# Optimization experiments

Measured on AMD Instinct MI355X. Metric: run time of the kernel, lower is better.

The kernel has to match this reference:

```python
import jax, jax.numpy as jnp
import numpy as np

N = 4096      # nodes
F = 512       # nfeat
D = 64        # nhid per head
H = 8         # nheads
C = 40        # nclass
ALPHA = 0.2   # leakyrelu slope
NEG = -1e9    # mask value (finite for bf16/fp16 safety; exp -> 0)
EDGE_P = 0.004


def setup_inputs() -> dict:
    key = jax.random.key(0)
    ks = jax.random.split(key, 8)
    x = jax.random.normal(ks[0], (N, F), jnp.float32)
    adj = jax.random.uniform(ks[1], (N, N)) < EDGE_P
    adj = adj | jnp.eye(N, dtype=bool)  # self-loops: every softmax row valid
    init = lambda k, shape, fan: jax.random.normal(k, shape, jnp.float32) / np.sqrt(fan)
    W1 = init(ks[2], (H, F, D), F)        # per-head tran.weight^T
    a1_src = init(ks[3], (H, D), D)       # att1 (j / source term)
    a1_dst = init(ks[4], (H, D), D)       # att2 (i / destination term)
    W2 = init(ks[5], (H * D, C), H * D)   # output head tran
    a2_src = init(ks[6], (C,), C)
    a2_dst = init(ks[7], (C,), C)
    return dict(x=x, adj=adj, W1=W1, a1_src=a1_src, a1_dst=a1_dst,
                W2=W2, a2_src=a2_src, a2_dst=a2_dst)


def reference(x, adj, W1, a1_src, a1_dst, W2, a2_src, a2_dst):
    # ---- layer 1: H heads in parallel (dropout = identity in eval) ----
    h = jnp.einsum('nf,hfd->hnd', x, W1)              # [H,N,D]
    si = jnp.einsum('hnd,hd->hn', h, a1_dst)          # att2(h): i term
    sj = jnp.einsum('hnd,hd->hn', h, a1_src)          # att1(h): j term
    e = jax.nn.leaky_relu(si[:, :, None] + sj[:, None, :], ALPHA)  # [H,N,N]
    e = jnp.where(adj[None], e, NEG)                  # mask non-edges
    p = jax.nn.softmax(e, axis=-1)                    # softmax over neighbors j
    out = jnp.einsum('hij,hjd->hid', p, h)            # [H,N,D]
    # torch.cat(heads, dim=1) -> [N, H*D] with heads contiguous
    x2 = jax.nn.elu(jnp.transpose(out, (1, 0, 2)).reshape(N, H * D))
    # ---- output attention head ----
    h2 = x2 @ W2                                      # [N,C]
    e2 = jax.nn.leaky_relu((h2 @ a2_dst)[:, None] + (h2 @ a2_src)[None, :], ALPHA)
    e2 = jnp.where(adj, e2, NEG)
    p2 = jax.nn.softmax(e2, axis=-1)
    return p2 @ h2                                    # [N,C]
```

## Files before the change

kernel.cpp:

```cpp
#include <hip/hip_runtime.h>

#define NN 4096
#define FF 512
#define DD 64
#define HH 8
#define CC 40
#define HD (HH * DD)
#define CP 64
#define MAXDEG 128
#define ALPHA 0.2f

#define BM 64
#define BN 64
#define BK 16
#define SK2 8
#define KH2 (FF / SK2)

typedef __attribute__((ext_vector_type(8))) short bf16x8;
typedef __attribute__((ext_vector_type(4))) float f32x4;

__device__ __forceinline__ float bf2f(unsigned short u) {
    union { unsigned int i; float f; } v;
    v.i = ((unsigned int)u) << 16;
    return v.f;
}

__device__ __forceinline__ unsigned short f2bf(float f) {
    union { float f; unsigned int u; } v;
    v.f = f;
    unsigned int r = v.u + 0x7fffu + ((v.u >> 16) & 1u);
    return (unsigned short)(r >> 16);
}

__device__ __forceinline__ float wave_sum(float v) {
    #pragma unroll
    for (int off = 32; off; off >>= 1) v += __shfl_xor(v, off, 64);
    return v;
}

__device__ __forceinline__ float wave_max(float v) {
    #pragma unroll
    for (int off = 32; off; off >>= 1) v = fmaxf(v, __shfl_xor(v, off, 64));
    return v;
}

__device__ __forceinline__ float read_f(const void* src, int i, int isBf16) {
    if (isBf16) return bf2f(((const unsigned short*)src)[i]);
    return ((const float*)src)[i];
}

__device__ __forceinline__ int sniff_x(const void* xraw, int tid, int* fS) {
    if (tid == 0) *fS = 1;
    __syncthreads();
    int bad = 0;
    const unsigned int* xw = (const unsigned int*)xraw;
    #pragma unroll
    for (int q = 0; q < 4; q++) {
        unsigned int w = xw[(tid & 255) * 4 + q];
        unsigned int e0 = (w >> 7) & 0xffu;
        unsigned int e1 = (w >> 23) & 0xffu;
        if (e0 >= 0x90u || e1 >= 0x90u) bad = 1;
    }
    if (bad) *fS = 0;
    __syncthreads();
    return *fS;
}

__global__ __launch_bounds__(256) void cvt_all(const void* __restrict__ x,
                                               const void* __restrict__ W1,
                                               const void* __restrict__ W2,
                                               const void* __restrict__ a1s,
                                               const void* __restrict__ a1d,
                                               const void* __restrict__ a2s,
                                               const void* __restrict__ a2d,
                                               unsigned short* __restrict__ W1bth,
                                               unsigned short* __restrict__ W1btl,
                                               float* __restrict__ W2p,
                                               float* __restrict__ a1sf,
                                               float* __restrict__ a1df,
                                               float* __restrict__ a2sf,
                                               float* __restrict__ a2df,
                                               float* __restrict__ si,
                                               float* __restrict__ sj) {
    __shared__ int fS;
    int bf = sniff_x(x, threadIdx.x, &fS);
    int i = blockIdx.x * 256 + threadIdx.x;
    const int nW1 = HH * FF * DD;
    const int nW2p = HD * CP;
    const int nA1 = HD;
    const int nSS = HH * NN;
    if (i < nW1) {
        int hd = i / (FF * DD);
        int rem = i % (FF * DD);
        int f = rem / DD, d = rem % DD;
        float v = read_f(W1, i, bf);
        unsigned short h16 = f2bf(v);
        int idx = (hd * DD + d) * FF + f;
        W1bth[idx] = h16;
        W1btl[idx] = f2bf(v - bf2f(h16));
        return;
    }
    i -= nW1;
    if (i < nW2p) {
        int k = i / CP, c = i % CP;
        W2p[i] = (c < CC) ? read_f(W2, k * CC + c, bf) : 0.f;
        return;
    }
    i -= nW2p;
    if (i < nA1) { a1sf[i] = read_f(a1s, i, bf); return; }
    i -= nA1;
    if (i < nA1) { a1df[i] = read_f(a1d, i, bf); return; }
    i -= nA1;
    if (i < CC) { a2sf[i] = read_f(a2s, i, bf); return; }
    i -= CC;
    if (i < CC) { a2df[i] = read_f(a2d, i, bf); return; }
    i -= CC;
    if (i < nSS) { si[i] = 0.f; return; }
    i -= nSS;
    if (i < nSS) { sj[i] = 0.f; return; }
}

__global__ __launch_bounds__(256) void build_nbr(const unsigned char* __restrict__ adj,
                                                 int* __restrict__ nbr,
                                                 int* __restrict__ deg) {
    __shared__ int cnt;
    __shared__ int fS;
    if (threadIdx.x == 0) { cnt = 0; fS = 1; }
    __syncthreads();
    if (adj[(size_t)threadIdx.x * (NN + 1)] == 0) fS = 0;
    __syncthreads();
    int isByte = fS;
    int i = blockIdx.x;
    if (isByte) {
        uint4 v = ((const uint4*)(adj + (size_t)i * NN))[threadIdx.x];
        unsigned int u[4] = { v.x, v.y, v.z, v.w };
        int base = threadIdx.x * 16;
        #pragma unroll
        for (int q = 0; q < 4; q++) {
            #pragma unroll
            for (int b = 0; b < 4; b++) {
                if ((u[q] >> (8 * b)) & 0xffu) {
                    int p = atomicAdd(&cnt, 1);
                    if (p < MAXDEG) nbr[(size_t)i * MAXDEG + p] = base + q * 4 + b;
                }
            }
        }
    } else {
        const int4* row = (const int4*)((const int*)adj + (size_t)i * NN);
        #pragma unroll
        for (int q = 0; q < 4; q++) {
            int idx4 = q * 256 + threadIdx.x;
            int4 v = row[idx4];
            int base = idx4 * 4;
            if (v.x) { int p = atomicAdd(&cnt, 1); if (p < MAXDEG) nbr[(size_t)i * MAXDEG + p] = base; }
            if (v.y) { int p = atomicAdd(&cnt, 1); if (p < MAXDEG) nbr[(size_t)i * MAXDEG + p] = base + 1; }
            if (v.z) { int p = atomicAdd(&cnt, 1); if (p < MAXDEG) nbr[(size_t)i * MAXDEG + p] = base + 2; }
            if (v.w) { int p = atomicAdd(&cnt, 1); if (p < MAXDEG) nbr[(size_t)i * MAXDEG + p] = base + 3; }
        }
    }
    __syncthreads();
    if (threadIdx.x == 0) deg[i] = min(cnt, MAXDEG);
}

__global__ __launch_bounds__(256) void l1_gemm(const void* __restrict__ xraw,
                                               const unsigned short* __restrict__ W1bth,
                                               const unsigned short* __restrict__ W1btl,
                                               const float* __restrict__ a1sf,
                                               const float* __restrict__ a1df,
                                               unsigned short* __restrict__ hb,
                                               float* __restrict__ si,
                                               float* __restrict__ sj) {
    __shared__ __align__(16) unsigned short Ah[64][40];
    __shared__ __align__(16) unsigned short Al[64][40];
    __shared__ __align__(16) unsigned short Bh[64][40];
    __shared__ __align__(16) unsigned short Bl[64][40];
    __shared__ int fS;

    int bm = blockIdx.x, hd = blockIdx.y;
    int tid = threadIdx.x;
    int isBf16 = sniff_x(xraw, tid, &fS);

    int wave = tid >> 6, lane = tid & 63;
    int wm = wave >> 1, wn = wave & 1;
    int lr = lane & 15, lg = lane >> 4;
    int srow = tid >> 2;
    int sseg = (tid & 3) * 8;

    const unsigned short* wAp = W1bth + (size_t)(hd * 64 + srow) * FF + sseg;
    const unsigned short* wBp = W1btl + (size_t)(hd * 64 + srow) * FF + sseg;

    f32x4 acc[2][2];
    #pragma unroll
    for (int r = 0; r < 2; r++)
        #pragma unroll
        for (int c = 0; c < 2; c++) acc[r][c] = (f32x4){0.f, 0.f, 0.f, 0.f};

    if (isBf16) {
        const unsigned short* xp = (const unsigned short*)xraw
                                 + (size_t)(bm * 64 + srow) * FF + sseg;
        uint4 ra = *(const uint4*)xp;
        uint4 rb = *(const uint4*)wAp;
        for (int kk = 0; kk < FF; kk += 32) {
            __syncthreads();
            *(uint4*)&Ah[srow][sseg] = ra;
            *(uint4*)&Bh[srow][sseg] = rb;
            __syncthreads();
            int kn = (kk + 32 < FF) ? kk + 32 : kk;
            ra = *(const uint4*)(xp + kn);
            rb = *(const uint4*)(wAp + kn);
            bf16x8 a0 = *(const bf16x8*)&Ah[wm * 32 + lr][lg * 8];
            bf16x8 a1 = *(const bf16x8*)&Ah[wm * 32 + 16 + lr][lg * 8];
            bf16x8 b0 = *(const bf16x8*)&Bh[wn * 32 + lr][lg * 8];
            bf16x8 b1 = *(const bf16x8*)&Bh[wn * 32 + 16 + lr][lg * 8];
            acc[0][0] = __builtin_amdgcn_mfma_f32_16x16x32_bf16(a0, b0, acc[0][0], 0, 0, 0);
            acc[0][1] = __builtin_amdgcn_mfma_f32_16x16x32_bf16(a0, b1, acc[0][1], 0, 0, 0);
            acc[1][0] = __builtin_amdgcn_mfma_f32_16x16x32_bf16(a1, b0, acc[1][0], 0, 0, 0);
            acc[1][1] = __builtin_amdgcn_mfma_f32_16x16x32_bf16(a1, b1, acc[1][1], 0, 0, 0);
        }
    } else {
        const float* xp = (const float*)xraw + (size_t)(bm * 64 + srow) * FF + sseg;
        float4 ra0 = *(const float4*)xp;
        float4 ra1 = *(const float4*)(xp + 4);
        uint4 rbh = *(const uint4*)wAp;
        uint4 rbl = *(const uint4*)wBp;
        for (int kk = 0; kk < FF; kk += 32) {
            __syncthreads();
            union { unsigned short s[8]; uint4 v; } uh, ul;
            float fv[8] = { ra0.x, ra0.y, ra0.z, ra0.w, ra1.x, ra1.y, ra1.z, ra1.w };
            #pragma unroll
            for (int q = 0; q < 8; q++) {
                unsigned short h16 = f2bf(fv[q]);
                uh.s[q] = h16;
                ul.s[q] = f2bf(fv[q] - bf2f(h16));
            }
            *(uint4*)&Ah[srow][sseg] = uh.v;
            *(uint4*)&Al[srow][sseg] = ul.v;
            *(uint4*)&Bh[srow][sseg] = rbh;
            *(uint4*)&Bl[srow][sseg] = rbl;
            __syncthreads();
            int kn = (kk + 32 < FF) ? kk + 32 : kk;
            ra0 = *(const float4*)(xp + kn);
            ra1 = *(const float4*)(xp + kn + 4);
            rbh = *(const uint4*)(wAp + kn);
            rbl = *(const uint4*)(wBp + kn);

            bf16x8 a_h0 = *(const bf16x8*)&Ah[wm * 32 + lr][lg * 8];
            bf16x8 a_h1 = *(const bf16x8*)&Ah[wm * 32 + 16 + lr][lg * 8];
            bf16x8 a_l0 = *(const bf16x8*)&Al[wm * 32 + lr][lg * 8];
            bf16x8 a_l1 = *(const bf16x8*)&Al[wm * 32 + 16 + lr][lg * 8];
            bf16x8 b_h0 = *(const bf16x8*)&Bh[wn * 32 + lr][lg * 8];
            bf16x8 b_h1 = *(const bf16x8*)&Bh[wn * 32 + 16 + lr][lg * 8];
            bf16x8 b_l0 = *(const bf16x8*)&Bl[wn * 32 + lr][lg * 8];
            bf16x8 b_l1 = *(const bf16x8*)&Bl[wn * 32 + 16 + lr][lg * 8];

            acc[0][0] = __builtin_amdgcn_mfma_f32_16x16x32_bf16(a_h0, b_h0, acc[0][0], 0, 0, 0);
            acc[0][1] = __builtin_amdgcn_mfma_f32_16x16x32_bf16(a_h0, b_h1, acc[0][1], 0, 0, 0);
            acc[1][0] = __builtin_amdgcn_mfma_f32_16x16x32_bf16(a_h1, b_h0, acc[1][0], 0, 0, 0);
            acc[1][1] = __builtin_amdgcn_mfma_f32_16x16x32_bf16(a_h1, b_h1, acc[1][1], 0, 0, 0);
            acc[0][0] = __builtin_amdgcn_mfma_f32_16x16x32_bf16(a_h0, b_l0, acc[0][0], 0, 0, 0);
            acc[0][1] = __builtin_amdgcn_mfma_f32_16x16x32_bf16(a_h0, b_l1, acc[0][1], 0, 0, 0);
            acc[1][0] = __builtin_amdgcn_mfma_f32_16x16x32_bf16(a_h1, b_l0, acc[1][0], 0, 0, 0);
            acc[1][1] = __builtin_amdgcn_mfma_f32_16x16x32_bf16(a_h1, b_l1, acc[1][1], 0, 0, 0);
            acc[0][0] = __builtin_amdgcn_mfma_f32_16x16x32_bf16(a_l0, b_h0, acc[0][0], 0, 0, 0);
            acc[0][1] = __builtin_amdgcn_mfma_f32_16x16x32_bf16(a_l0, b_h1, acc[0][1], 0, 0, 0);
            acc[1][0] = __builtin_amdgcn_mfma_f32_16x16x32_bf16(a_l1, b_h0, acc[1][0], 0, 0, 0);
            acc[1][1] = __builtin_amdgcn_mfma_f32_16x16x32_bf16(a_l1, b_h1, acc[1][1], 0, 0, 0);
        }
    }

    float adv[2], asv[2];
    #pragma unroll
    for (int fc = 0; fc < 2; fc++) {
        adv[fc] = a1df[hd * DD + wn * 32 + fc * 16 + lr];
        asv[fc] = a1sf[hd * DD + wn * 32 + fc * 16 + lr];
    }
    #pragma unroll
    for (int fr = 0; fr < 2; fr++) {
        #pragma unroll
        for (int q = 0; q < 4; q++) {
            int row = bm * 64 + wm * 32 + fr * 16 + lg * 4 + q;
            int colb = hd * 64 + wn * 32;
            hb[(size_t)row * HD + colb + lr] = f2bf(acc[fr][0][q]);
            hb[(size_t)row * HD + colb + 16 + lr] = f2bf(acc[fr][1][q]);
            float pd = acc[fr][0][q] * adv[0] + acc[fr][1][q] * adv[1];
            float ps = acc[fr][0][q] * asv[0] + acc[fr][1][q] * asv[1];
            #pragma unroll
            for (int off = 1; off < 16; off <<= 1) {
                pd += __shfl_xor(pd, off, 64);
                ps += __shfl_xor(ps, off, 64);
            }
            if (lr == 0) {
                atomicAdd(&si[hd * NN + row], pd);
                atomicAdd(&sj[hd * NN + row], ps);
            }
        }
    }
}

__global__ __launch_bounds__(256) void l1_attn(const int* __restrict__ nbr,
                                               const int* __restrict__ deg,
                                               const unsigned short* __restrict__ hb,
                                               const float* __restrict__ si,
                                               const float* __restrict__ sj,
                                               float* __restrict__ x2) {
    int i = blockIdx.x;
    int tid = threadIdx.x;
    int wave = tid >> 6, lane = tid & 63;
    int d = deg[i];
    __shared__ int js[MAXDEG];
    __shared__ float wls[HH][MAXDEG];
    for (int k = tid; k < d; k += 256) js[k] = nbr[(size_t)i * MAXDEG + k];
    __syncthreads();

    int hd = wave * 2 + (lane >> 5);
    int l32 = lane & 31;
    float sii = si[hd * NN + i];
    const float* sjh = sj + (size_t)hd * NN;
    float m = -1e30f;
    for (int k = l32; k < d; k += 32) {
        float sc = sii + sjh[js[k]];
        sc = sc > 0.f ? sc : ALPHA * sc;
        wls[hd][k] = sc;
        m = fmaxf(m, sc);
    }
    #pragma unroll
    for (int off = 16; off; off >>= 1) m = fmaxf(m, __shfl_xor(m, off, 64));
    float s = 0.f;
    for (int k = l32; k < d; k += 32) {
        float e = expf(wls[hd][k] - m);
        wls[hd][k] = e;
        s += e;
    }
    #pragma unroll
    for (int off = 16; off; off >>= 1) s += __shfl_xor(s, off, 64);
    float inv = 1.f / fmaxf(s, 1e-30f);
    for (int k = l32; k < d; k += 32) wls[hd][k] *= inv;
    __syncthreads();

    const unsigned int* hu = (const unsigned int*)hb;
    const float* wl = wls[tid >> 5];
    float a0 = 0.f, a1 = 0.f;
    int k = 0;
    for (; k + 4 <= d; k += 4) {
        unsigned int v0 = hu[(size_t)js[k] * 256 + tid];
        unsigned int v1 = hu[(size_t)js[k + 1] * 256 + tid];
        unsigned int v2 = hu[(size_t)js[k + 2] * 256 + tid];
        unsigned int v3 = hu[(size_t)js[k + 3] * 256 + tid];
        float w0 = wl[k], w1 = wl[k + 1], w2 = wl[k + 2], w3 = wl[k + 3];
        a0 = fmaf(w0, bf2f((unsigned short)v0), a0);
        a1 = fmaf(w0, bf2f((unsigned short)(v0 >> 16)), a1);
        a0 = fmaf(w1, bf2f((unsigned short)v1), a0);
        a1 = fmaf(w1, bf2f((unsigned short)(v1 >> 16)), a1);
        a0 = fmaf(w2, bf2f((unsigned short)v2), a0);
        a1 = fmaf(w2, bf2f((unsigned short)(v2 >> 16)), a1);
        a0 = fmaf(w3, bf2f((unsigned short)v3), a0);
        a1 = fmaf(w3, bf2f((unsigned short)(v3 >> 16)), a1);
    }
    for (; k < d; k++) {
        unsigned int v = hu[(size_t)js[k] * 256 + tid];
        float w = wl[k];
        a0 = fmaf(w, bf2f((unsigned short)v), a0);
        a1 = fmaf(w, bf2f((unsigned short)(v >> 16)), a1);
    }
    float r0 = a0 > 0.f ? a0 : expm1f(a0);
    float r1 = a1 > 0.f ? a1 : expm1f(a1);
    *(float2*)(x2 + (size_t)i * HD + tid * 2) = make_float2(r0, r1);
}

template <int KHs, int Nb>
__device__ __forceinline__ void gemm_body(const float* __restrict__ Ap,
                                          const float* __restrict__ Bp,
                                          float* __restrict__ Co,
                                          int tid, int bm) {
    __shared__ float As[BK][BM + 4];
    __shared__ float Bs[BK][BN + 4];
    int tm = tid >> 4, tn = tid & 15;
    int m0 = tm * 4, n0 = tn * 4;
    int ar = tid >> 2, ak = (tid & 3) * 4;
    int bk = tid >> 4, bq = (tid & 15) * 4;

    float acc[4][4];
    #pragma unroll
    for (int r = 0; r < 4; r++)
        #pragma unroll
        for (int c = 0; c < 4; c++) acc[r][c] = 0.f;

    const float* Ar = Ap + (size_t)ar * FF;
    float4 av = *(const float4*)(Ar + ak);
    float4 bv = *(const float4*)(Bp + (size_t)bk * Nb + bq);

    for (int k0 = 0; k0 < KHs; k0 += BK) {
        __syncthreads();
        As[ak + 0][ar] = av.x;
        As[ak + 1][ar] = av.y;
        As[ak + 2][ar] = av.z;
        As[ak + 3][ar] = av.w;
        *(float4*)&Bs[bk][bq] = bv;
        __syncthreads();

        int kn = (k0 + BK < KHs) ? k0 + BK : k0;
        av = *(const float4*)(Ar + kn + ak);
        bv = *(const float4*)(Bp + (size_t)(kn + bk) * Nb + bq);

        #pragma unroll
        for (int k = 0; k < BK; k++) {
            float4 a = *(const float4*)&As[k][m0];
            float4 b = *(const float4*)&Bs[k][n0];
            acc[0][0] = fmaf(a.x, b.x, acc[0][0]);
            acc[0][1] = fmaf(a.x, b.y, acc[0][1]);
            acc[0][2] = fmaf(a.x, b.z, acc[0][2]);
            acc[0][3] = fmaf(a.x, b.w, acc[0][3]);
            acc[1][0] = fmaf(a.y, b.x, acc[1][0]);
            acc[1][1] = fmaf(a.y, b.y, acc[1][1]);
            acc[1][2] = fmaf(a.y, b.z, acc[1][2]);
            acc[1][3] = fmaf(a.y, b.w, acc[1][3]);
            acc[2][0] = fmaf(a.z, b.x, acc[2][0]);
            acc[2][1] = fmaf(a.z, b.y, acc[2][1]);
            acc[2][2] = fmaf(a.z, b.z, acc[2][2]);
            acc[2][3] = fmaf(a.z, b.w, acc[2][3]);
            acc[3][0] = fmaf(a.w, b.x, acc[3][0]);
            acc[3][1] = fmaf(a.w, b.y, acc[3][1]);
            acc[3][2] = fmaf(a.w, b.z, acc[3][2]);
            acc[3][3] = fmaf(a.w, b.w, acc[3][3]);
        }
    }

    #pragma unroll
    for (int r = 0; r < 4; r++) {
        float4 v = make_float4(acc[r][0], acc[r][1], acc[r][2], acc[r][3]);
        *(float4*)(Co + (size_t)(bm * BM + m0 + r) * Nb + n0) = v;
    }
}

__global__ __launch_bounds__(256) void l2_gemm(const float* __restrict__ x2,
                                               const float* __restrict__ W2p,
                                               float* __restrict__ Cp2) {
    int bm = blockIdx.x, sk = blockIdx.z;
    gemm_body<KH2, CP>(x2 + (size_t)bm * BM * FF + sk * KH2,
                       W2p + (size_t)(sk * KH2) * CP,
                       Cp2 + (size_t)sk * NN * CP,
                       threadIdx.x, bm);
}

__global__ __launch_bounds__(64) void l2_post(const float* __restrict__ Cp2,
                                              const float* __restrict__ a2sf,
                                              const float* __restrict__ a2df,
                                              float* __restrict__ h2,
                                              float* __restrict__ d1,
                                              float* __restrict__ d2) {
    int n = blockIdx.x, c = threadIdx.x;
    float v = 0.f;
    #pragma unroll
    for (int sk = 0; sk < SK2; sk++)
        v += Cp2[(size_t)sk * NN * CP + (size_t)n * CP + c];
    if (c < CC) h2[(size_t)n * CC + c] = v;
    float pd = wave_sum((c < CC) ? v * a2df[c] : 0.f);
    float ps = wave_sum((c < CC) ? v * a2sf[c] : 0.f);
    if (c == 0) {
        d1[n] = pd;
        d2[n] = ps;
    }
}

__global__ __launch_bounds__(256) void l2_attn(const int* __restrict__ nbr,
                                               const int* __restrict__ deg,
                                               const float* __restrict__ h2,
                                               const float* __restrict__ d1,
                                               const float* __restrict__ d2,
                                               float* __restrict__ out) {
    int w = threadIdx.x >> 6, lane = threadIdx.x & 63;
    int i = blockIdx.x * 4 + w;
    int d = deg[i];
    __shared__ int js[4][MAXDEG];
    __shared__ float wls[4][MAXDEG];
    for (int k = lane; k < d; k += 64) js[w][k] = nbr[(size_t)i * MAXDEG + k];

    float sii = d1[i];
    float m = -1e30f;
    for (int k = lane; k < d; k += 64) {
        float sc = sii + d2[js[w][k]];
        sc = sc > 0.f ? sc : ALPHA * sc;
        wls[w][k] = sc;
        m = fmaxf(m, sc);
    }
    m = wave_max(m);
    float s = 0.f;
    for (int k = lane; k < d; k += 64) {
        float e = expf(wls[w][k] - m);
        wls[w][k] = e;
        s += e;
    }
    s = fmaxf(wave_sum(s), 1e-30f);

    int c = lane;
    if (c < CC) {
        float acc = 0.f;
        int k = 0;
        for (; k + 4 <= d; k += 4) {
            float v0 = h2[(size_t)js[w][k] * CC + c];
            float v1 = h2[(size_t)js[w][k + 1] * CC + c];
            float v2 = h2[(size_t)js[w][k + 2] * CC + c];
            float v3 = h2[(size_t)js[w][k + 3] * CC + c];
            acc = fmaf(wls[w][k], v0, acc);
            acc = fmaf(wls[w][k + 1], v1, acc);
            acc = fmaf(wls[w][k + 2], v2, acc);
            acc = fmaf(wls[w][k + 3], v3, acc);
        }
        for (; k < d; k++)
            acc = fmaf(wls[w][k], h2[(size_t)js[w][k] * CC + c], acc);
        out[(size_t)i * CC + c] = acc / s;
    }
}

extern "C" void kernel_launch(void* const* d_in, const int* in_sizes, int n_in,
                              void* d_out, int out_size, void* d_ws, size_t ws_size,
                              hipStream_t stream) {
    const void* x   = d_in[0];
    const unsigned char* adj = (const unsigned char*)d_in[1];
    const void* W1  = d_in[2];
    const void* a1s = d_in[3];
    const void* a1d = d_in[4];
    const void* W2  = d_in[5];
    const void* a2s = d_in[6];
    const void* a2d = d_in[7];

    char* ws = (char*)d_ws;
    int*   nbr   = (int*)(ws + 0);
    int*   deg   = (int*)(ws + 2097152);
    float* si    = (float*)(ws + 2113536);
    float* sj    = (float*)(ws + 2244608);
    unsigned short* W1bth = (unsigned short*)(ws + 2375680);
    unsigned short* W1btl = (unsigned short*)(ws + 2899968);
    float* W2p   = (float*)(ws + 3424256);
    float* a1sf  = (float*)(ws + 3555328);
    float* a1df  = (float*)(ws + 3557376);
    float* a2sf  = (float*)(ws + 3559424);
    float* a2df  = (float*)(ws + 3559680);
    unsigned short* hb = (unsigned short*)(ws + 3559936);
    float* x2    = (float*)(ws + 7754240);
    float* h2    = (float*)(ws + 16142848);
    float* d1    = (float*)(ws + 16798208);
    float* d2    = (float*)(ws + 16814592);
    float* Cp2   = (float*)(ws + 16830976);

    const int nCvt = HH * FF * DD + HD * CP + 2 * HD + 2 * CC + 2 * HH * NN;
    hipLaunchKernelGGL(cvt_all, dim3((nCvt + 255) / 256), dim3(256), 0, stream,
                       x, W1, W2, a1s, a1d, a2s, a2d,
                       W1bth, W1btl, W2p, a1sf, a1df, a2sf, a2df, si, sj);

    hipLaunchKernelGGL(build_nbr, dim3(NN), dim3(256), 0, stream, adj, nbr, deg);
    hipLaunchKernelGGL(l1_gemm, dim3(NN / 64, HH), dim3(256), 0, stream,
                       x, W1bth, W1btl, a1sf, a1df, hb, si, sj);
    hipLaunchKernelGGL(l1_attn, dim3(NN), dim3(256), 0, stream,
                       nbr, deg, hb, si, sj, x2);
    hipLaunchKernelGGL(l2_gemm, dim3(NN / BM, 1, SK2), dim3(256), 0, stream,
                       x2, W2p, Cp2);
    hipLaunchKernelGGL(l2_post, dim3(NN), dim3(64), 0, stream,
                       Cp2, a2sf, a2df, h2, d1, d2);
    hipLaunchKernelGGL(l2_attn, dim3(NN / 4), dim3(256), 0, stream,
                       nbr, deg, h2, d1, d2, (float*)d_out);
}
```

Measured before the change: 166.5 us.

## Merge conversion and neighbor-build kernels; replace si/sj atomics with LDS reduction

Merges the weight-conversion kernel and the adjacency neighbor-list kernel into one prep launch. The W1 transpose-split is reorganized so each thread handles 16 contiguous output features. In the layer-1 GEMM epilogue, the two column-wave partial dot products are combined through shared memory and written directly, replacing global atomics. This also removes the need to zero si/sj. The aims are to cut a launch, drop the zero-fill work and avoid atomic traffic, at the cost of an extra block barrier and a more varied prep grid.

```diff
diff --git a/kernel.cpp b/kernel.cpp
--- a/kernel.cpp
+++ b/kernel.cpp
@@ -66,41 +66,94 @@
     return *fS;
 }
 
-__global__ __launch_bounds__(256) void cvt_all(const void* __restrict__ x,
-                                               const void* __restrict__ W1,
-                                               const void* __restrict__ W2,
-                                               const void* __restrict__ a1s,
-                                               const void* __restrict__ a1d,
-                                               const void* __restrict__ a2s,
-                                               const void* __restrict__ a2d,
-                                               unsigned short* __restrict__ W1bth,
-                                               unsigned short* __restrict__ W1btl,
-                                               float* __restrict__ W2p,
-                                               float* __restrict__ a1sf,
-                                               float* __restrict__ a1df,
-                                               float* __restrict__ a2sf,
-                                               float* __restrict__ a2df,
-                                               float* __restrict__ si,
-                                               float* __restrict__ sj) {
+__global__ __launch_bounds__(256) void prep(const unsigned char* __restrict__ adj,
+                                            const void* __restrict__ x,
+                                            const void* __restrict__ W1,
+                                            const void* __restrict__ W2,
+                                            const void* __restrict__ a1s,
+                                            const void* __restrict__ a1d,
+                                            const void* __restrict__ a2s,
+                                            const void* __restrict__ a2d,
+                                            int* __restrict__ nbr,
+                                            int* __restrict__ deg,
+                                            unsigned short* __restrict__ W1bth,
+                                            unsigned short* __restrict__ W1btl,
+                                            float* __restrict__ W2p,
+                                            float* __restrict__ a1sf,
+                                            float* __restrict__ a1df,
+                                            float* __restrict__ a2sf,
+                                            float* __restrict__ a2df) {
+    __shared__ int cnt;
     __shared__ int fS;
-    int bf = sniff_x(x, threadIdx.x, &fS);
-    int i = blockIdx.x * 256 + threadIdx.x;
-    const int nW1 = HH * FF * DD;
+    int t = threadIdx.x;
+    int blk = blockIdx.x;
+
+    if (blk < NN) {
+        if (t == 0) { cnt = 0; fS = 1; }
+        __syncthreads();
+        if (adj[(size_t)t * (NN + 1)] == 0) fS = 0;
+        __syncthreads();
+        int isByte = fS;
+        int i = blk;
+        if (isByte) {
+            uint4 v = ((const uint4*)(adj + (size_t)i * NN))[t];
+            unsigned int u[4] = { v.x, v.y, v.z, v.w };
+            int base = t * 16;
+            #pragma unroll
+            for (int q = 0; q < 4; q++) {
+                #pragma unroll
+                for (int b = 0; b < 4; b++) {
+                    if ((u[q] >> (8 * b)) & 0xffu) {
+                        int p = atomicAdd(&cnt, 1);
+                        if (p < MAXDEG) nbr[(size_t)i * MAXDEG + p] = base + q * 4 + b;
+                    }
+                }
+            }
+        } else {
+            const int4* row = (const int4*)((const int*)adj + (size_t)i * NN);
+            #pragma unroll
+            for (int q = 0; q < 4; q++) {
+                int idx4 = q * 256 + t;
+                int4 v = row[idx4];
+                int base = idx4 * 4;
+                if (v.x) { int p = atomicAdd(&cnt, 1); if (p < MAXDEG) nbr[(size_t)i * MAXDEG + p] = base; }
+                if (v.y) { int p = atomicAdd(&cnt, 1); if (p < MAXDEG) nbr[(size_t)i * MAXDEG + p] = base + 1; }
+                if (v.z) { int p = atomicAdd(&cnt, 1); if (p < MAXDEG) nbr[(size_t)i * MAXDEG + p] = base + 2; }
+                if (v.w) { int p = atomicAdd(&cnt, 1); if (p < MAXDEG) nbr[(size_t)i * MAXDEG + p] = base + 3; }
+            }
+        }
+        __syncthreads();
+        if (t == 0) deg[i] = min(cnt, MAXDEG);
+        return;
+    }
+
+    int bf = sniff_x(x, t, &fS);
+
+    if (blk < NN + 64) {
+        int b = blk - NN;
+        int ob = b * 4096 + t * 16;
+        int row = ob >> 9;
+        int f0 = ob & 511;
+        int hd = row >> 6, d = row & 63;
+        unsigned short hi[16], lo[16];
+        #pragma unroll
+        for (int q = 0; q < 16; q++) {
+            float v = read_f(W1, (hd * FF + f0 + q) * DD + d, bf);
+            unsigned short h16 = f2bf(v);
+            hi[q] = h16;
+            lo[q] = f2bf(v - bf2f(h16));
+        }
+        #pragma unroll
+        for (int q = 0; q < 16; q++) {
+            W1bth[(size_t)row * FF + f0 + q] = hi[q];
+            W1btl[(size_t)row * FF + f0 + q] = lo[q];
+        }
+        return;
+    }
+
+    int i = (blk - NN - 64) * 256 + t;
     const int nW2p = HD * CP;
     const int nA1 = HD;
-    const int nSS = HH * NN;
-    if (i < nW1) {
-        int hd = i / (FF * DD);
-        int rem = i % (FF * DD);
-        int f = rem / DD, d = rem % DD;
-        float v = read_f(W1, i, bf);
-        unsigned short h16 = f2bf(v);
-        int idx = (hd * DD + d) * FF + f;
-        W1bth[idx] = h16;
-        W1btl[idx] = f2bf(v - bf2f(h16));
-        return;
-    }
-    i -= nW1;
     if (i < nW2p) {
         int k = i / CP, c = i % CP;
         W2p[i] = (c < CC) ? read_f(W2, k * CC + c, bf) : 0.f;
@@ -114,52 +167,6 @@
     if (i < CC) { a2sf[i] = read_f(a2s, i, bf); return; }
     i -= CC;
     if (i < CC) { a2df[i] = read_f(a2d, i, bf); return; }
-    i -= CC;
-    if (i < nSS) { si[i] = 0.f; return; }
-    i -= nSS;
-    if (i < nSS) { sj[i] = 0.f; return; }
-}
-
-__global__ __launch_bounds__(256) void build_nbr(const unsigned char* __restrict__ adj,
-                                                 int* __restrict__ nbr,
-                                                 int* __restrict__ deg) {
-    __shared__ int cnt;
-    __shared__ int fS;
-    if (threadIdx.x == 0) { cnt = 0; fS = 1; }
-    __syncthreads();
-    if (adj[(size_t)threadIdx.x * (NN + 1)] == 0) fS = 0;
-    __syncthreads();
-    int isByte = fS;
-    int i = blockIdx.x;
-    if (isByte) {
-        uint4 v = ((const uint4*)(adj + (size_t)i * NN))[threadIdx.x];
-        unsigned int u[4] = { v.x, v.y, v.z, v.w };
-        int base = threadIdx.x * 16;
-        #pragma unroll
-        for (int q = 0; q < 4; q++) {
-            #pragma unroll
-            for (int b = 0; b < 4; b++) {
-                if ((u[q] >> (8 * b)) & 0xffu) {
-                    int p = atomicAdd(&cnt, 1);
-                    if (p < MAXDEG) nbr[(size_t)i * MAXDEG + p] = base + q * 4 + b;
-                }
-            }
-        }
-    } else {
-        const int4* row = (const int4*)((const int*)adj + (size_t)i * NN);
-        #pragma unroll
-        for (int q = 0; q < 4; q++) {
-            int idx4 = q * 256 + threadIdx.x;
-            int4 v = row[idx4];
-            int base = idx4 * 4;
-            if (v.x) { int p = atomicAdd(&cnt, 1); if (p < MAXDEG) nbr[(size_t)i * MAXDEG + p] = base; }
-            if (v.y) { int p = atomicAdd(&cnt, 1); if (p < MAXDEG) nbr[(size_t)i * MAXDEG + p] = base + 1; }
-            if (v.z) { int p = atomicAdd(&cnt, 1); if (p < MAXDEG) nbr[(size_t)i * MAXDEG + p] = base + 2; }
-            if (v.w) { int p = atomicAdd(&cnt, 1); if (p < MAXDEG) nbr[(size_t)i * MAXDEG + p] = base + 3; }
-        }
-    }
-    __syncthreads();
-    if (threadIdx.x == 0) deg[i] = min(cnt, MAXDEG);
 }
 
 __global__ __launch_bounds__(256) void l1_gemm(const void* __restrict__ xraw,
@@ -274,6 +281,7 @@
         adv[fc] = a1df[hd * DD + wn * 32 + fc * 16 + lr];
         asv[fc] = a1sf[hd * DD + wn * 32 + fc * 16 + lr];
     }
+    float pdv[2][4], psv[2][4];
     #pragma unroll
     for (int fr = 0; fr < 2; fr++) {
         #pragma unroll
@@ -289,11 +297,33 @@
                 pd += __shfl_xor(pd, off, 64);
                 ps += __shfl_xor(ps, off, 64);
             }
-            if (lr == 0) {
-                atomicAdd(&si[hd * NN + row], pd);
-                atomicAdd(&sj[hd * NN + row], ps);
+            pdv[fr][q] = pd;
+            psv[fr][q] = ps;
+        }
+    }
+    float* sred = (float*)&Ah[0][0];
+    __syncthreads();
+    if (wn == 0 && lr == 0) {
+        #pragma unroll
+        for (int fr = 0; fr < 2; fr++)
+            #pragma unroll
+            for (int q = 0; q < 4; q++) {
+                int rl = wm * 32 + fr * 16 + lg * 4 + q;
+                sred[rl * 2] = pdv[fr][q];
+                sred[rl * 2 + 1] = psv[fr][q];
             }
-        }
+    }
+    __syncthreads();
+    if (wn == 1 && lr == 0) {
+        #pragma unroll
+        for (int fr = 0; fr < 2; fr++)
+            #pragma unroll
+            for (int q = 0; q < 4; q++) {
+                int rl = wm * 32 + fr * 16 + lg * 4 + q;
+                int row = bm * 64 + rl;
+                si[hd * NN + row] = sred[rl * 2] + pdv[fr][q];
+                sj[hd * NN + row] = sred[rl * 2 + 1] + psv[fr][q];
+            }
     }
 }
 
@@ -543,12 +573,12 @@
     float* d2    = (float*)(ws + 16814592);
     float* Cp2   = (float*)(ws + 16830976);
 
-    const int nCvt = HH * FF * DD + HD * CP + 2 * HD + 2 * CC + 2 * HH * NN;
-    hipLaunchKernelGGL(cvt_all, dim3((nCvt + 255) / 256), dim3(256), 0, stream,
-                       x, W1, W2, a1s, a1d, a2s, a2d,
-                       W1bth, W1btl, W2p, a1sf, a1df, a2sf, a2df, si, sj);
-
-    hipLaunchKernelGGL(build_nbr, dim3(NN), dim3(256), 0, stream, adj, nbr, deg);
+    const int nSmall = HD * CP + 2 * HD + 2 * CC;
+    const int prepGrid = NN + 64 + (nSmall + 255) / 256;
+    hipLaunchKernelGGL(prep, dim3(prepGrid), dim3(256), 0, stream,
+                       adj, x, W1, W2, a1s, a1d, a2s, a2d,
+                       nbr, deg, W1bth, W1btl, W2p, a1sf, a1df, a2sf, a2df);
+
     hipLaunchKernelGGL(l1_gemm, dim3(NN / 64, HH), dim3(256), 0, stream,
                        x, W1bth, W1btl, a1sf, a1df, hb, si, sj);
     hipLaunchKernelGGL(l1_attn, dim3(NN), dim3(256), 0, stream,
```

After: 160.8 us (median of 2 runs). -3.4%, faster.
